# Optimization experiments

Hardware: AMD Instinct MI355X
Metric: run time of the kernel (lower is better)

The kernel has to match this reference:

```python
import jax
import jax.numpy as jnp
import numpy as np

N = 256   # hardcoded in the torch module via expand(256, 256)
D = 256
K = 16
M_MARGIN = 0.6
T_THRESH = 0.0025
EPS = 1e-12


def setup_inputs() -> dict:
    key = jax.random.key(0)
    k1, k2 = jax.random.split(key)
    yi = jax.random.normal(k1, (N, D), dtype=jnp.float32)
    yi_t = jax.random.normal(k2, (N, D), dtype=jnp.float32)
    return {"yi": yi, "yi_t": yi_t}


def _l2_normalize(x):
    return x / jnp.sqrt(jnp.sum(x * x, axis=-1, keepdims=True) + EPS)


def reference(yi, yi_t):
    yi_n = _l2_normalize(yi)      # [N, D]
    yit_n = _l2_normalize(yi_t)   # [N, D]

    # pairwise half-distances: [N, N]
    diff = yi_n[:, None, :] - yi_n[None, :, :]           # [N, N, D]
    dis_yii = 0.5 * jnp.sqrt(jnp.sum(diff * diff, axis=-1) + EPS)

    # K+1 smallest distances per row (self is smallest)
    neg_vals, topk_idx = jax.lax.top_k(-dis_yii, K + 1)  # [N, K+1]
    nbr_idx = topk_idx[:, 1:]                            # [N, K] exclude self

    yj = yi_n[nbr_idx]                                   # [N, K, D]
    dis_yij = 0.5 * jnp.sqrt(jnp.sum((yi_n[:, None, :] - yj) ** 2, axis=-1) + EPS)
    dis_yi_tj = 0.5 * jnp.sqrt(jnp.sum((yit_n[:, None, :] - yj) ** 2, axis=-1) + EPS)

    e1 = jnp.sum((dis_yij - dis_yi_tj) ** 2 - T_THRESH)

    # margin term: dist(yi, yi_t) + m - (second smallest pairwise dist)
    dis_yi_yi_t = 0.5 * jnp.sqrt(jnp.sum((yi_n - yit_n) ** 2, axis=-1) + EPS)  # [N]
    second_nn = -neg_vals[:, 1]                          # [N]
    out = dis_yi_yi_t + M_MARGIN - second_nn
    e2 = jnp.sum(jnp.maximum(out, 0.0))

    return e1 + e2
```

## Files before the change

kernel.cpp:

```cpp
#include <hip/hip_runtime.h>
#include <math.h>

#define NN 256
#define DD 256
#define KK 16
#define M_MARGIN 0.6f
#define T_THRESH 0.0025f
#define EPS 1e-12f

__global__ void __launch_bounds__(1024) blcd_row_kernel(
    const float* __restrict__ yi, const float* __restrict__ yit,
    float* __restrict__ partial)
{
    __shared__ float s_yi[DD];
    __shared__ float s_yit[DD];
    __shared__ float sdis[NN];
    __shared__ float red[48];

    const int i = blockIdx.x;
    const int t = threadIdx.x;
    const int j = t >> 2;
    const int s = t & 3;
    const int w = t >> 6;

    float a = 0.0f, b = 0.0f;
    if (t < DD) {
        a = yi [i * DD + t];
        b = yit[i * DD + t];
    }

    const float4* __restrict__ rj = (const float4*)(yi + j * DD);
    float4 p[16];
    #pragma unroll
    for (int k = 0; k < 16; ++k) p[k] = rj[4 * k + s];

    if (t < DD) { s_yi[t] = a; s_yit[t] = b; }

    float r0 = a * a, r1 = b * b, r2 = a * b;
    #pragma unroll
    for (int off = 32; off > 0; off >>= 1) {
        r0 += __shfl_down(r0, off, 64);
        r1 += __shfl_down(r1, off, 64);
        r2 += __shfl_down(r2, off, 64);
    }
    if ((t & 63) == 0) { red[w] = r0; red[16 + w] = r1; red[32 + w] = r2; }
    __syncthreads();

    const float nn_i  = (red[0]  + red[1])  + (red[2]  + red[3]);
    const float nn_it = (red[16] + red[17]) + (red[18] + red[19]);
    const float cross = (red[32] + red[33]) + (red[34] + red[35]);
    const float inv_ni  = 1.0f / sqrtf(nn_i  + EPS);
    const float inv_nit = 1.0f / sqrtf(nn_it + EPS);

    const float4* __restrict__ si  = (const float4*)s_yi;
    const float4* __restrict__ sit = (const float4*)s_yit;
    float4 q4  = make_float4(0.f, 0.f, 0.f, 0.f);
    float4 qt4 = make_float4(0.f, 0.f, 0.f, 0.f);
    float4 nn4 = make_float4(0.f, 0.f, 0.f, 0.f);
    #pragma unroll
    for (int k = 0; k < 16; ++k) {
        const int d4 = 4 * k + s;
        float4 y = p[k];
        float4 u = si[d4];
        float4 v = sit[d4];
        q4.x  += y.x * u.x; q4.y  += y.y * u.y; q4.z  += y.z * u.z; q4.w  += y.w * u.w;
        qt4.x += y.x * v.x; qt4.y += y.y * v.y; qt4.z += y.z * v.z; qt4.w += y.w * v.w;
        nn4.x += y.x * y.x; nn4.y += y.y * y.y; nn4.z += y.z * y.z; nn4.w += y.w * y.w;
    }
    float q  = (q4.x  + q4.y ) + (q4.z  + q4.w );
    float qt = (qt4.x + qt4.y) + (qt4.z + qt4.w);
    float nn = (nn4.x + nn4.y) + (nn4.z + nn4.w);
    q  += __shfl_xor(q,  1, 64);  q  += __shfl_xor(q,  2, 64);
    qt += __shfl_xor(qt, 1, 64);  qt += __shfl_xor(qt, 2, 64);
    nn += __shfl_xor(nn, 1, 64);  nn += __shfl_xor(nn, 2, 64);

    const float inv_nt = 1.0f / sqrtf(nn + EPS);
    const float c    = q  * inv_nt * inv_ni;
    const float ct   = qt * inv_nt * inv_nit;
    const float myv  = 0.5f * sqrtf(fmaxf(2.0f - 2.0f * c , 0.0f) + EPS);
    const float myvt = 0.5f * sqrtf(fmaxf(2.0f - 2.0f * ct, 0.0f) + EPS);
    if (s == 0) sdis[j] = myv;
    __syncthreads();

    int rank = 0;
    const float4* sd4 = (const float4*)sdis;
    #pragma unroll
    for (int m = 0; m < 16; ++m) {
        const int k = 4 * m + s;
        float4 v = sd4[k];
        const int jj = k * 4;
        rank += (v.x < myv || (v.x == myv && (jj + 0) < j)) ? 1 : 0;
        rank += (v.y < myv || (v.y == myv && (jj + 1) < j)) ? 1 : 0;
        rank += (v.z < myv || (v.z == myv && (jj + 2) < j)) ? 1 : 0;
        rank += (v.w < myv || (v.w == myv && (jj + 3) < j)) ? 1 : 0;
    }
    rank += __shfl_xor(rank, 1, 64);
    rank += __shfl_xor(rank, 2, 64);

    float contrib = 0.0f;
    if (s == 0) {
        if (rank >= 1 && rank <= KK) {
            const float dd = myv - myvt;
            contrib = dd * dd - T_THRESH;
        }
        if (rank == 1) {
            const float cc = cross * inv_ni * inv_nit;
            const float d_iit = 0.5f * sqrtf(fmaxf(2.0f - 2.0f * cc, 0.0f) + EPS);
            contrib += fmaxf(d_iit + M_MARGIN - myv, 0.0f);
        }
    }

    #pragma unroll
    for (int off = 32; off > 0; off >>= 1) contrib += __shfl_down(contrib, off, 64);
    if ((t & 63) == 0) red[w] = contrib;
    __syncthreads();
    if (t == 0) {
        float tot = ((red[0]  + red[1])  + (red[2]  + red[3]))
                  + ((red[4]  + red[5])  + (red[6]  + red[7]))
                  + ((red[8]  + red[9])  + (red[10] + red[11]))
                  + ((red[12] + red[13]) + (red[14] + red[15]));
        partial[i] = tot;
    }
}

__global__ void __launch_bounds__(NN) blcd_reduce_kernel(
    const float* __restrict__ partial, float* __restrict__ out)
{
    __shared__ float red[4];
    const int t = threadIdx.x;
    float v = partial[t];
    #pragma unroll
    for (int off = 32; off > 0; off >>= 1) v += __shfl_down(v, off, 64);
    if ((t & 63) == 0) red[t >> 6] = v;
    __syncthreads();
    if (t == 0) out[0] = (red[0] + red[1]) + (red[2] + red[3]);
}

extern "C" void kernel_launch(void* const* d_in, const int* in_sizes, int n_in,
                              void* d_out, int out_size, void* d_ws, size_t ws_size,
                              hipStream_t stream) {
    (void)in_sizes; (void)n_in; (void)out_size; (void)ws_size;

    const float* yi  = (const float*)d_in[0];
    const float* yit = (const float*)d_in[1];
    float* out = (float*)d_out;
    float* ws  = (float*)d_ws;

    blcd_row_kernel<<<NN, 1024, 0, stream>>>(yi, yit, ws);
    blcd_reduce_kernel<<<1, NN, 0, stream>>>(ws, out);
}
```

Measured before the change: 64.30 us.

## Defer yi_t dot products to top-k neighbours and shrink final reduction

The row kernel no longer computes yi_t dot products for all 256 candidate rows. It first computes only the yi distances and ranks, then computes the yi_t and cross products just for the 16 selected neighbours. The block-wide norm reduction through shared memory and its extra sync are replaced by per-thread norm accumulation in the main loop. The final reduce kernel now uses one 64-thread wave reading float4 values and has no shared memory; the divergent neighbour branch adds a second pass over shared data for the selected lanes.

```diff
diff --git a/kernel.cpp b/kernel.cpp
--- a/kernel.cpp
+++ b/kernel.cpp
@@ -15,7 +15,7 @@
     __shared__ float s_yi[DD];
     __shared__ float s_yit[DD];
     __shared__ float sdis[NN];
-    __shared__ float red[48];
+    __shared__ float red[16];
 
     const int i = blockIdx.x;
     const int t = threadIdx.x;
@@ -23,10 +23,9 @@
     const int s = t & 3;
     const int w = t >> 6;
 
-    float a = 0.0f, b = 0.0f;
     if (t < DD) {
-        a = yi [i * DD + t];
-        b = yit[i * DD + t];
+        s_yi[t]  = yi [i * DD + t];
+        s_yit[t] = yit[i * DD + t];
     }
 
     const float4* __restrict__ rj = (const float4*)(yi + j * DD);
@@ -34,51 +33,31 @@
     #pragma unroll
     for (int k = 0; k < 16; ++k) p[k] = rj[4 * k + s];
 
-    if (t < DD) { s_yi[t] = a; s_yit[t] = b; }
-
-    float r0 = a * a, r1 = b * b, r2 = a * b;
-    #pragma unroll
-    for (int off = 32; off > 0; off >>= 1) {
-        r0 += __shfl_down(r0, off, 64);
-        r1 += __shfl_down(r1, off, 64);
-        r2 += __shfl_down(r2, off, 64);
-    }
-    if ((t & 63) == 0) { red[w] = r0; red[16 + w] = r1; red[32 + w] = r2; }
     __syncthreads();
 
-    const float nn_i  = (red[0]  + red[1])  + (red[2]  + red[3]);
-    const float nn_it = (red[16] + red[17]) + (red[18] + red[19]);
-    const float cross = (red[32] + red[33]) + (red[34] + red[35]);
-    const float inv_ni  = 1.0f / sqrtf(nn_i  + EPS);
-    const float inv_nit = 1.0f / sqrtf(nn_it + EPS);
-
-    const float4* __restrict__ si  = (const float4*)s_yi;
-    const float4* __restrict__ sit = (const float4*)s_yit;
+    const float4* __restrict__ si = (const float4*)s_yi;
     float4 q4  = make_float4(0.f, 0.f, 0.f, 0.f);
-    float4 qt4 = make_float4(0.f, 0.f, 0.f, 0.f);
     float4 nn4 = make_float4(0.f, 0.f, 0.f, 0.f);
+    float4 uu4 = make_float4(0.f, 0.f, 0.f, 0.f);
     #pragma unroll
     for (int k = 0; k < 16; ++k) {
-        const int d4 = 4 * k + s;
-        float4 y = p[k];
-        float4 u = si[d4];
-        float4 v = sit[d4];
+        const float4 y = p[k];
+        const float4 u = si[4 * k + s];
         q4.x  += y.x * u.x; q4.y  += y.y * u.y; q4.z  += y.z * u.z; q4.w  += y.w * u.w;
-        qt4.x += y.x * v.x; qt4.y += y.y * v.y; qt4.z += y.z * v.z; qt4.w += y.w * v.w;
         nn4.x += y.x * y.x; nn4.y += y.y * y.y; nn4.z += y.z * y.z; nn4.w += y.w * y.w;
+        uu4.x += u.x * u.x; uu4.y += u.y * u.y; uu4.z += u.z * u.z; uu4.w += u.w * u.w;
     }
     float q  = (q4.x  + q4.y ) + (q4.z  + q4.w );
-    float qt = (qt4.x + qt4.y) + (qt4.z + qt4.w);
     float nn = (nn4.x + nn4.y) + (nn4.z + nn4.w);
+    float uu = (uu4.x + uu4.y) + (uu4.z + uu4.w);
     q  += __shfl_xor(q,  1, 64);  q  += __shfl_xor(q,  2, 64);
-    qt += __shfl_xor(qt, 1, 64);  qt += __shfl_xor(qt, 2, 64);
     nn += __shfl_xor(nn, 1, 64);  nn += __shfl_xor(nn, 2, 64);
+    uu += __shfl_xor(uu, 1, 64);  uu += __shfl_xor(uu, 2, 64);
 
+    const float inv_ni = 1.0f / sqrtf(uu + EPS);
     const float inv_nt = 1.0f / sqrtf(nn + EPS);
-    const float c    = q  * inv_nt * inv_ni;
-    const float ct   = qt * inv_nt * inv_nit;
-    const float myv  = 0.5f * sqrtf(fmaxf(2.0f - 2.0f * c , 0.0f) + EPS);
-    const float myvt = 0.5f * sqrtf(fmaxf(2.0f - 2.0f * ct, 0.0f) + EPS);
+    const float c   = q * inv_nt * inv_ni;
+    const float myv = 0.5f * sqrtf(fmaxf(2.0f - 2.0f * c, 0.0f) + EPS);
     if (s == 0) sdis[j] = myv;
     __syncthreads();
 
@@ -98,15 +77,38 @@
     rank += __shfl_xor(rank, 2, 64);
 
     float contrib = 0.0f;
-    if (s == 0) {
-        if (rank >= 1 && rank <= KK) {
+    if (rank >= 1 && rank <= KK) {
+        const float4* __restrict__ sit = (const float4*)s_yit;
+        float4 qt4 = make_float4(0.f, 0.f, 0.f, 0.f);
+        float4 vv4 = make_float4(0.f, 0.f, 0.f, 0.f);
+        float4 uv4 = make_float4(0.f, 0.f, 0.f, 0.f);
+        #pragma unroll
+        for (int k = 0; k < 16; ++k) {
+            const float4 y = p[k];
+            const float4 u = si [4 * k + s];
+            const float4 v = sit[4 * k + s];
+            qt4.x += y.x * v.x; qt4.y += y.y * v.y; qt4.z += y.z * v.z; qt4.w += y.w * v.w;
+            vv4.x += v.x * v.x; vv4.y += v.y * v.y; vv4.z += v.z * v.z; vv4.w += v.w * v.w;
+            uv4.x += u.x * v.x; uv4.y += u.y * v.y; uv4.z += u.z * v.z; uv4.w += u.w * v.w;
+        }
+        float qt = (qt4.x + qt4.y) + (qt4.z + qt4.w);
+        float vv = (vv4.x + vv4.y) + (vv4.z + vv4.w);
+        float uv = (uv4.x + uv4.y) + (uv4.z + uv4.w);
+        qt += __shfl_xor(qt, 1, 64);  qt += __shfl_xor(qt, 2, 64);
+        vv += __shfl_xor(vv, 1, 64);  vv += __shfl_xor(vv, 2, 64);
+        uv += __shfl_xor(uv, 1, 64);  uv += __shfl_xor(uv, 2, 64);
+
+        const float inv_nit = 1.0f / sqrtf(vv + EPS);
+        const float ct   = qt * inv_nt * inv_nit;
+        const float myvt = 0.5f * sqrtf(fmaxf(2.0f - 2.0f * ct, 0.0f) + EPS);
+        if (s == 0) {
             const float dd = myv - myvt;
             contrib = dd * dd - T_THRESH;
-        }
-        if (rank == 1) {
-            const float cc = cross * inv_ni * inv_nit;
-            const float d_iit = 0.5f * sqrtf(fmaxf(2.0f - 2.0f * cc, 0.0f) + EPS);
-            contrib += fmaxf(d_iit + M_MARGIN - myv, 0.0f);
+            if (rank == 1) {
+                const float cc = uv * inv_ni * inv_nit;
+                const float d_iit = 0.5f * sqrtf(fmaxf(2.0f - 2.0f * cc, 0.0f) + EPS);
+                contrib += fmaxf(d_iit + M_MARGIN - myv, 0.0f);
+            }
         }
     }
 
@@ -123,17 +125,15 @@
     }
 }
 
-__global__ void __launch_bounds__(NN) blcd_reduce_kernel(
+__global__ void __launch_bounds__(64) blcd_reduce_kernel(
     const float* __restrict__ partial, float* __restrict__ out)
 {
-    __shared__ float red[4];
     const int t = threadIdx.x;
-    float v = partial[t];
+    const float4 v4 = ((const float4*)partial)[t];
+    float v = (v4.x + v4.y) + (v4.z + v4.w);
     #pragma unroll
     for (int off = 32; off > 0; off >>= 1) v += __shfl_down(v, off, 64);
-    if ((t & 63) == 0) red[t >> 6] = v;
-    __syncthreads();
-    if (t == 0) out[0] = (red[0] + red[1]) + (red[2] + red[3]);
+    if (t == 0) out[0] = v;
 }
 
 extern "C" void kernel_launch(void* const* d_in, const int* in_sizes, int n_in,
@@ -147,5 +147,5 @@
     float* ws  = (float*)d_ws;
 
     blcd_row_kernel<<<NN, 1024, 0, stream>>>(yi, yit, ws);
-    blcd_reduce_kernel<<<1, NN, 0, stream>>>(ws, out);
+    blcd_reduce_kernel<<<1, 64, 0, stream>>>(ws, out);
 }
```

New measurement: 64.55 us. Within noise of the previous version (+0.4%).
